# Kernel tuning notes

Measured on AMD Instinct MI355X. Metric: run time of the kernel, lower is better.

Reference implementation:

```python
import jax, jax.numpy as jnp
import numpy as np

N_NODES = 100000
N_EDGES = 1600000
N_GRAPHS = 512
IN_DIM = 128
HID = 128
N_CLASSES = 10


def _gcn_conv(x, W, b, src, dst, n):
    """PyG GCNConv: out = D^{-1/2} (A+I) D^{-1/2} (x @ W) + b."""
    xw = x @ W  # [n, out_dim]
    loop = jnp.arange(n)
    s = jnp.concatenate([src, loop])  # add self loops
    d = jnp.concatenate([dst, loop])
    deg = jax.ops.segment_sum(jnp.ones(s.shape, dtype=xw.dtype), d, num_segments=n)
    dinv = jnp.where(deg > 0, jax.lax.rsqrt(deg), jnp.zeros((), xw.dtype))
    norm = dinv[s] * dinv[d]  # [E + n]
    out = jax.ops.segment_sum(xw[s] * norm[:, None], d, num_segments=n)
    return out + b


def _global_mean_pool(x, batch, num_graphs):
    sums = jax.ops.segment_sum(x, batch, num_segments=num_graphs)
    cnts = jax.ops.segment_sum(jnp.ones(batch.shape, dtype=x.dtype), batch, num_segments=num_graphs)
    return sums / jnp.maximum(cnts, 1.0)[:, None]


def setup_inputs() -> dict:
    key = jax.random.key(0)
    ks = jax.random.split(key, 8)
    x = jax.random.normal(ks[0], (N_NODES, IN_DIM), dtype=jnp.float32)
    edge_index = jax.random.randint(ks[1], (2, N_EDGES), 0, N_NODES, dtype=jnp.int64)
    batch = jnp.sort(jax.random.randint(ks[2], (N_NODES,), 0, N_GRAPHS, dtype=jnp.int64))
    sc = 1.0 / np.sqrt(IN_DIM)
    W1 = jax.random.normal(ks[3], (IN_DIM, HID), dtype=jnp.float32) * sc
    b1 = jnp.zeros((HID,), dtype=jnp.float32)
    W2 = jax.random.normal(ks[4], (HID, HID), dtype=jnp.float32) * (1.0 / np.sqrt(HID))
    b2 = jnp.zeros((HID,), dtype=jnp.float32)
    Wc = jax.random.normal(ks[5], (HID, N_CLASSES), dtype=jnp.float32) * (1.0 / np.sqrt(HID))
    bc = jnp.zeros((N_CLASSES,), dtype=jnp.float32)
    return {"x": x, "edge_index": edge_index, "batch": batch,
            "W1": W1, "b1": b1, "W2": W2, "b2": b2, "Wc": Wc, "bc": bc}


def reference(x, edge_index, batch, W1, b1, W2, b2, Wc, bc):
    src, dst = edge_index[0], edge_index[1]
    n = x.shape[0]
    h = _gcn_conv(x, W1, b1, src, dst, n)
    h = jax.nn.relu(h)
    h = _gcn_conv(h, W2, b2, src, dst, n)
    g = _global_mean_pool(h, batch, N_GRAPHS)
    return g @ Wc + bc
```

## Files before the change

### kernel.cpp

```cpp
#include <hip/hip_runtime.h>

#define N_NODES 100000
#define N_EDGES 1600000
#define N_GRAPHS 512
#define DIM 128
#define NCLS 10
#define NBKT 782
#define BCAP 2560

typedef __attribute__((ext_vector_type(8))) short short8;
typedef __attribute__((ext_vector_type(4))) float f32x4;

static __device__ __forceinline__ unsigned short f2bf(float f) {
    unsigned u = __float_as_uint(f);
    unsigned r = (u + 0x7FFF + ((u >> 16) & 1)) >> 16;
    return (unsigned short)r;
}
static __device__ __forceinline__ float bf2f(unsigned u) {
    return __uint_as_float(u << 16);
}


__global__ void k_wprep(const float* __restrict__ W1, const float* __restrict__ W2,
                        unsigned short* __restrict__ wf1, unsigned short* __restrict__ wf2,
                        int* __restrict__ bcnt) {
    int b = blockIdx.x;
    if (b >= 128) {
        int i = (b - 128) * 256 + threadIdx.x;
        if (i < NBKT) bcnt[i] = 0;
        return;
    }
    const float* W = (b < 64) ? W1 : W2;
    unsigned short* wfrag = (b < 64) ? wf1 : wf2;
    int t = (b & 63) * 256 + threadIdx.x;
    int j = t & 7, lane = (t >> 3) & 63, nt = (t >> 9) & 7, kit = t >> 12;
    int k = kit * 32 + (lane >> 4) * 8 + j;
    int n = nt * 16 + (lane & 15);
    float v = W[k * 128 + n];
    unsigned short h = f2bf(v);
    wfrag[t] = h;
    wfrag[16384 + t] = f2bf(v - bf2f(h));
}


__global__ __launch_bounds__(256) void k_bucket(
    const int* __restrict__ src, const int* __restrict__ dst,
    int* __restrict__ bcnt, unsigned* __restrict__ bpack, int E) {
    __shared__ int cnt[NBKT];
    __shared__ int base[NBKT];
    int tid = threadIdx.x;
    for (int i = tid; i < NBKT; i += 256) cnt[i] = 0;
    __syncthreads();
    int e0 = blockIdx.x * 4096 + tid;
    unsigned pk[16]; short bk[16];
#pragma unroll
    for (int j = 0; j < 16; j++) {
        int e = e0 + j * 256;
        if (e < E) {
            int s = src[e], d = dst[e];
            bk[j] = (short)(d >> 7);
            pk[j] = ((unsigned)(d & 127) << 17) | (unsigned)s;
            atomicAdd(&cnt[bk[j]], 1);
        } else bk[j] = -1;
    }
    __syncthreads();
    for (int i = tid; i < NBKT; i += 256) {
        int c = cnt[i];
        base[i] = c ? atomicAdd(&bcnt[i], c) : 0;
        cnt[i] = 0;
    }
    __syncthreads();
#pragma unroll
    for (int j = 0; j < 16; j++) {
        if (bk[j] >= 0) {
            int p = base[bk[j]] + atomicAdd(&cnt[bk[j]], 1);
            if (p < BCAP) bpack[(size_t)bk[j] * BCAP + p] = pk[j];
        }
    }
}


static __device__ __forceinline__ void bsort_body(
    char* smemraw, int b,
    const unsigned* __restrict__ bpack, const int* __restrict__ bcnt,
    int* __restrict__ rp, float* __restrict__ dinv,
    int* __restrict__ esrc, int N, float* __restrict__ dvs) {
    int* lds      = (int*)smemraw;
    int* cnt      = lds + 256;
    int* scan     = lds + 384;
    int* cur      = lds + 512;
    int* gbase_sh = lds + 640;
    int tid = threadIdx.x;
    int v[4], pre[4];
    int s = 0;
#pragma unroll
    for (int j = 0; j < 4; j++) {
        int idx = tid * 4 + j;
        v[j] = (idx < NBKT) ? min(bcnt[idx], BCAP) : 0;
        pre[j] = s; s += v[j];
    }
    lds[tid] = s;
    __syncthreads();
    for (int off = 1; off < 256; off <<= 1) {
        int t = (tid >= off) ? lds[tid - off] : 0;
        __syncthreads();
        lds[tid] += t;
        __syncthreads();
    }
    if (tid == (b >> 2)) *gbase_sh = lds[tid] - s + pre[b & 3];
    if (tid < 128) cnt[tid] = 0;
    __syncthreads();
    int gbase = *gbase_sh;
    int n0 = b << 7;
    int m = min(bcnt[b], BCAP);
    const unsigned* bp = bpack + (size_t)b * BCAP;
    for (int j = tid; j < m; j += 256) atomicAdd(&cnt[bp[j] >> 17], 1);
    __syncthreads();
    if (tid < 128) scan[tid] = cnt[tid];
    __syncthreads();
    for (int off = 1; off < 128; off <<= 1) {
        int t = (tid < 128 && tid >= off) ? scan[tid - off] : 0;
        __syncthreads();
        if (tid < 128) scan[tid] += t;
        __syncthreads();
    }
    if (tid < 128) {
        int c = cnt[tid];
        int excl = scan[tid] - c;
        int node = n0 + tid;
        float dv = rsqrtf((float)(c + 1));
        if (node <= N) rp[node] = gbase + excl;
        if (node < N) dinv[node] = dv;
        dvs[tid] = dv;
        cur[tid] = gbase + excl;
    }
    __syncthreads();
    for (int j = tid; j < m; j += 256) {
        unsigned pk = bp[j];
        int p = atomicAdd(&cur[pk >> 17], 1);
        esrc[p] = (int)(pk & 0x1FFFF);
    }
}

static __device__ __forceinline__ void gemm_f32_body(
    char* smemraw, int rowBlk,
    const float* __restrict__ A, const unsigned short* __restrict__ wfrag,
    const float* __restrict__ dvs, unsigned short* __restrict__ ybf, int M) {
    unsigned short* ldsw = (unsigned short*)smemraw;
    int tid = threadIdx.x, wave = tid >> 6, lane = tid & 63;
    int m = lane & 15, quad = lane >> 4;
    int rowBase = rowBlk * 128 + wave * 32;
    int r0 = rowBase + m, r1 = rowBase + 16 + m;
    for (int i = tid; i < 2048; i += 256)
        ((short8*)ldsw)[i] = ((const short8*)wfrag)[i];
    __syncthreads();
    f32x4 acc0[8], acc1[8];
#pragma unroll
    for (int i = 0; i < 8; i++) { acc0[i] = (f32x4){0,0,0,0}; acc1[i] = (f32x4){0,0,0,0}; }
    const unsigned short* wlo = wfrag + 16384;

#pragma unroll
    for (int kit = 0; kit < 4; kit++) {
        float a0[8], a1[8];
        if (r0 < M) {
            const float4* ap = (const float4*)(A + (size_t)r0 * 128 + kit * 32 + quad * 8);
            float4 f0 = ap[0], f1 = ap[1];
            a0[0]=f0.x; a0[1]=f0.y; a0[2]=f0.z; a0[3]=f0.w; a0[4]=f1.x; a0[5]=f1.y; a0[6]=f1.z; a0[7]=f1.w;
        } else { for (int j = 0; j < 8; j++) a0[j] = 0.f; }
        if (r1 < M) {
            const float4* ap = (const float4*)(A + (size_t)r1 * 128 + kit * 32 + quad * 8);
            float4 f0 = ap[0], f1 = ap[1];
            a1[0]=f0.x; a1[1]=f0.y; a1[2]=f0.z; a1[3]=f0.w; a1[4]=f1.x; a1[5]=f1.y; a1[6]=f1.z; a1[7]=f1.w;
        } else { for (int j = 0; j < 8; j++) a1[j] = 0.f; }
        short8 ahi0, alo0, ahi1, alo1;
#pragma unroll
        for (int j = 0; j < 8; j++) {
            unsigned short h0 = f2bf(a0[j]);
            ahi0[j] = (short)h0; alo0[j] = (short)f2bf(a0[j] - bf2f(h0));
            unsigned short h1 = f2bf(a1[j]);
            ahi1[j] = (short)h1; alo1[j] = (short)f2bf(a1[j] - bf2f(h1));
        }
        int fb = kit * 4096 + lane * 8;
#pragma unroll
        for (int nt = 0; nt < 8; nt++) {
            int idx = fb + nt * 512;
            short8 bhi = *(const short8*)(ldsw + idx);
            short8 blo = *(const short8*)(wlo + idx);
            acc0[nt] = __builtin_amdgcn_mfma_f32_16x16x32_bf16(ahi0, bhi, acc0[nt], 0, 0, 0);
            acc0[nt] = __builtin_amdgcn_mfma_f32_16x16x32_bf16(alo0, bhi, acc0[nt], 0, 0, 0);
            acc0[nt] = __builtin_amdgcn_mfma_f32_16x16x32_bf16(ahi0, blo, acc0[nt], 0, 0, 0);
            acc1[nt] = __builtin_amdgcn_mfma_f32_16x16x32_bf16(ahi1, bhi, acc1[nt], 0, 0, 0);
            acc1[nt] = __builtin_amdgcn_mfma_f32_16x16x32_bf16(alo1, bhi, acc1[nt], 0, 0, 0);
            acc1[nt] = __builtin_amdgcn_mfma_f32_16x16x32_bf16(ahi1, blo, acc1[nt], 0, 0, 0);
        }
    }
    __syncthreads();
    unsigned short* wsm = ldsw + wave * 32 * 136;
#pragma unroll
    for (int rg = 0; rg < 4; rg++) {
        float s0 = dvs[wave * 32 + quad * 4 + rg];
        float s1 = dvs[wave * 32 + 16 + quad * 4 + rg];
#pragma unroll
        for (int nt = 0; nt < 8; nt++) {
            wsm[(quad * 4 + rg) * 136 + nt * 16 + m] = f2bf(acc0[nt][rg] * s0);
            wsm[(16 + quad * 4 + rg) * 136 + nt * 16 + m] = f2bf(acc1[nt][rg] * s1);
        }
    }
    __syncthreads();
#pragma unroll
    for (int i = 0; i < 8; i++) {
        int rl = i * 4 + quad;
        int grow = rowBase + rl;
        if (grow < M) {
            short8 v = *(const short8*)(wsm + rl * 136 + m * 8);
            *(short8*)(ybf + (size_t)grow * 128 + m * 8) = v;
        }
    }
}


__global__ __launch_bounds__(256) void k_fuse(
    const unsigned* __restrict__ bpack, const int* __restrict__ bcnt,
    int* __restrict__ rp, float* __restrict__ dinv, int* __restrict__ esrc, int N,
    const float* __restrict__ A, const unsigned short* __restrict__ wfrag,
    unsigned short* __restrict__ ybf, int M) {
    __shared__ __align__(16) char smem[4 * 32 * 136 * 2];
    __shared__ float dvs[128];
    int b = blockIdx.x;
    bsort_body(smem, b, bpack, bcnt, rp, dinv, esrc, N, dvs);
    __syncthreads();
    gemm_f32_body(smem, b, A, wfrag, dvs, ybf, M);
}


__global__ __launch_bounds__(256) void k_gemm_bf(
    const unsigned short* __restrict__ A, const unsigned short* __restrict__ wfrag,
    const float* __restrict__ dinv, unsigned short* __restrict__ ybf, int M) {
    __shared__ unsigned short ldsw[4 * 32 * 136];
    int tid = threadIdx.x, wave = tid >> 6, lane = tid & 63;
    int m = lane & 15, quad = lane >> 4;
    int rowBase = blockIdx.x * 128 + wave * 32;
    int r0 = rowBase + m, r1 = rowBase + 16 + m;
    for (int i = tid; i < 2048; i += 256)
        ((short8*)ldsw)[i] = ((const short8*)wfrag)[i];
    __syncthreads();
    f32x4 acc0[8], acc1[8];
#pragma unroll
    for (int i = 0; i < 8; i++) { acc0[i] = (f32x4){0,0,0,0}; acc1[i] = (f32x4){0,0,0,0}; }
    const unsigned short* wlo = wfrag + 16384;

#pragma unroll
    for (int kit = 0; kit < 4; kit++) {
        short8 ah0, ah1;
        if (r0 < M) ah0 = *(const short8*)(A + (size_t)r0 * 128 + kit * 32 + quad * 8);
        else { for (int j = 0; j < 8; j++) ah0[j] = 0; }
        if (r1 < M) ah1 = *(const short8*)(A + (size_t)r1 * 128 + kit * 32 + quad * 8);
        else { for (int j = 0; j < 8; j++) ah1[j] = 0; }
        int fb = kit * 4096 + lane * 8;
#pragma unroll
        for (int nt = 0; nt < 8; nt++) {
            int idx = fb + nt * 512;
            short8 bhi = *(const short8*)(ldsw + idx);
            short8 blo = *(const short8*)(wlo + idx);
            acc0[nt] = __builtin_amdgcn_mfma_f32_16x16x32_bf16(ah0, bhi, acc0[nt], 0, 0, 0);
            acc0[nt] = __builtin_amdgcn_mfma_f32_16x16x32_bf16(ah0, blo, acc0[nt], 0, 0, 0);
            acc1[nt] = __builtin_amdgcn_mfma_f32_16x16x32_bf16(ah1, bhi, acc1[nt], 0, 0, 0);
            acc1[nt] = __builtin_amdgcn_mfma_f32_16x16x32_bf16(ah1, blo, acc1[nt], 0, 0, 0);
        }
    }
    __syncthreads();
    float dv0 = (r0 < M) ? dinv[r0] : 0.f;
    float dv1 = (r1 < M) ? dinv[r1] : 0.f;
    unsigned short* wsm = ldsw + wave * 32 * 136;
#pragma unroll
    for (int rg = 0; rg < 4; rg++) {
        float s0 = __shfl(dv0, quad * 4 + rg);
        float s1 = __shfl(dv1, quad * 4 + rg);
#pragma unroll
        for (int nt = 0; nt < 8; nt++) {
            wsm[(quad * 4 + rg) * 136 + nt * 16 + m] = f2bf(acc0[nt][rg] * s0);
            wsm[(16 + quad * 4 + rg) * 136 + nt * 16 + m] = f2bf(acc1[nt][rg] * s1);
        }
    }
    __syncthreads();
#pragma unroll
    for (int i = 0; i < 8; i++) {
        int rl = i * 4 + quad;
        int grow = rowBase + rl;
        if (grow < M) {
            short8 v = *(const short8*)(wsm + rl * 136 + m * 8);
            *(short8*)(ybf + (size_t)grow * 128 + m * 8) = v;
        }
    }
}


__global__ __launch_bounds__(256) void k_agg(
    const unsigned short* __restrict__ y, const float* __restrict__ dinv,
    const int* __restrict__ rp, const int* __restrict__ esrc,
    const float* __restrict__ bias, unsigned* __restrict__ out, int relu, int N) {
    int wave = threadIdx.x >> 6;
    int lane = threadIdx.x & 63;
    int node = blockIdx.x * 4 + wave;
    if (node >= N) return;
    const unsigned* y2 = (const unsigned*)y;
    unsigned vs = y2[(size_t)node * 64 + lane];
    float a0 = bf2f(vs & 0xFFFF), a1 = bf2f(vs >> 16);
    int beg = rp[node], end = rp[node + 1];
    int j = beg;
    while (j < end) {
        int idxv = (j + lane < end) ? esrc[j + lane] : 0;
        int cnt = end - j; if (cnt > 64) cnt = 64;
        int i = 0;
        for (; i + 4 <= cnt; i += 4) {
            int s0 = __shfl(idxv, i + 0);
            int s1 = __shfl(idxv, i + 1);
            int s2 = __shfl(idxv, i + 2);
            int s3 = __shfl(idxv, i + 3);
            unsigned v0 = y2[(size_t)s0 * 64 + lane];
            unsigned v1 = y2[(size_t)s1 * 64 + lane];
            unsigned v2 = y2[(size_t)s2 * 64 + lane];
            unsigned v3 = y2[(size_t)s3 * 64 + lane];
            a0 += bf2f(v0 & 0xFFFF); a1 += bf2f(v0 >> 16);
            a0 += bf2f(v1 & 0xFFFF); a1 += bf2f(v1 >> 16);
            a0 += bf2f(v2 & 0xFFFF); a1 += bf2f(v2 >> 16);
            a0 += bf2f(v3 & 0xFFFF); a1 += bf2f(v3 >> 16);
        }
        for (; i < cnt; i++) {
            int s = __shfl(idxv, i);
            unsigned v = y2[(size_t)s * 64 + lane];
            a0 += bf2f(v & 0xFFFF); a1 += bf2f(v >> 16);
        }
        j += cnt;
    }
    float s = dinv[node];
    float2 bv = ((const float2*)bias)[lane];
    float o0 = s * a0 + bv.x;
    float o1 = s * a1 + bv.y;
    if (relu) { o0 = fmaxf(o0, 0.f); o1 = fmaxf(o1, 0.f); }
    out[(size_t)node * 64 + lane] = (unsigned)f2bf(o0) | ((unsigned)f2bf(o1) << 16);
}


__global__ __launch_bounds__(256) void k_poolhead(
    const unsigned* __restrict__ h2, const int* __restrict__ batch,
    const float* __restrict__ Wc, const float* __restrict__ bc,
    float* __restrict__ out, int n) {
    __shared__ float2 red[4][64];
    __shared__ float grow[DIM];
    int gid = blockIdx.x;
    int tid = threadIdx.x, wave = tid >> 6, lane = tid & 63;
    int lo = 0, hi = n;
    while (lo < hi) { int mid = (lo + hi) >> 1; if (batch[mid] < gid) lo = mid + 1; else hi = mid; }
    int start = lo;
    hi = n;
    while (lo < hi) { int mid = (lo + hi) >> 1; if (batch[mid] < gid + 1) lo = mid + 1; else hi = mid; }
    int end = lo;
    float a0 = 0.f, a1 = 0.f;
    for (int r = start + wave; r < end; r += 4) {
        unsigned v = h2[(size_t)r * 64 + lane];
        a0 += bf2f(v & 0xFFFF); a1 += bf2f(v >> 16);
    }
    red[wave][lane] = make_float2(a0, a1);
    __syncthreads();
    if (tid < 64) {
        float2 s = red[0][tid];
        s.x += red[1][tid].x; s.y += red[1][tid].y;
        s.x += red[2][tid].x; s.y += red[2][tid].y;
        s.x += red[3][tid].x; s.y += red[3][tid].y;
        int cnt = end - start;
        float inv = 1.f / (float)(cnt > 0 ? cnt : 1);
        grow[tid * 2] = s.x * inv;
        grow[tid * 2 + 1] = s.y * inv;
    }
    __syncthreads();
    if (tid < NCLS) {
        float acc = bc[tid];
#pragma unroll 16
        for (int k = 0; k < DIM; k++) acc += grow[k] * Wc[k * NCLS + tid];
        out[gid * NCLS + tid] = acc;
    }
}

extern "C" void kernel_launch(void* const* d_in, const int* in_sizes, int n_in,
                              void* d_out, int out_size, void* d_ws, size_t ws_size,
                              hipStream_t stream) {
    const float* x    = (const float*)d_in[0];
    const int*   ei   = (const int*)d_in[1];
    const int*   batch= (const int*)d_in[2];
    const float* W1   = (const float*)d_in[3];
    const float* b1   = (const float*)d_in[4];
    const float* W2   = (const float*)d_in[5];
    const float* b2   = (const float*)d_in[6];
    const float* Wc   = (const float*)d_in[7];
    const float* bc   = (const float*)d_in[8];
    float* out = (float*)d_out;
    const int N = N_NODES, E = N_EDGES;
    const int* src = ei;
    const int* dst = ei + E;

    char* ws = (char*)d_ws;
    size_t off = 0;
    auto carve = [&](size_t bytes) -> void* {
        void* p = ws + off;
        off = (off + bytes + 255) & ~(size_t)255;
        return p;
    };
    int*      rp    = (int*)     carve((size_t)(N + 1) * 4);
    float*    dinv  = (float*)   carve((size_t)N * 4);
    int*      bcnt  = (int*)     carve(NBKT * 4);
    unsigned* bpack = (unsigned*)carve((size_t)NBKT * BCAP * 4);
    int*      esrc  = (int*)     carve((size_t)E * 4);
    unsigned short* wf1 = (unsigned short*)carve(2 * 16384 * 2);
    unsigned short* wf2 = (unsigned short*)carve(2 * 16384 * 2);
    unsigned short* bufY = (unsigned short*)carve((size_t)N * DIM * 2);
    unsigned short* bufH = (unsigned short*)carve((size_t)N * DIM * 2);
    (void)ws_size; (void)n_in; (void)in_sizes; (void)out_size;

    const int nbBkt = (E + 4095) / 4096;
    const int gemmGrid = (N + 127) / 128;

    hipLaunchKernelGGL(k_wprep,  dim3(128 + (NBKT + 255) / 256), dim3(256), 0, stream, W1, W2, wf1, wf2, bcnt);
    hipLaunchKernelGGL(k_bucket, dim3(nbBkt), dim3(256), 0, stream, src, dst, bcnt, bpack, E);
    hipLaunchKernelGGL(k_fuse, dim3(NBKT), dim3(256), 0, stream,
                       bpack, bcnt, rp, dinv, esrc, N, x, wf1, bufY, N);
    hipLaunchKernelGGL(k_agg, dim3((N + 3) / 4), dim3(256), 0, stream, bufY, dinv, rp, esrc, b1, (unsigned*)bufH, 1, N);
    hipLaunchKernelGGL(k_gemm_bf, dim3(gemmGrid), dim3(256), 0, stream, bufH, wf2, dinv, bufY, N);
    hipLaunchKernelGGL(k_agg, dim3((N + 3) / 4), dim3(256), 0, stream, bufY, dinv, rp, esrc, b2, (unsigned*)bufH, 0, N);
    hipLaunchKernelGGL(k_poolhead, dim3(N_GRAPHS), dim3(256), 0, stream, (const unsigned*)bufH, batch, Wc, bc, out, N);
}
```

Measured before the change: 337.7 us.

## Fuse layer-1 aggregation with layer-2 GEMM in one slab kernel

Replaces the separate layer-1 aggregation kernel and the layer-2 bf16 GEMM with one kernel. Each block of 8 waves gathers neighbor features for 128 nodes, applies bias and ReLU, and writes the rows to LDS as bf16. The same block then runs the MFMA GEMM against W2 straight from LDS and scales each row by dinv. This removes a global write and read of the hidden activation and one launch. In exchange, the irregular gather and the GEMM are serialized within a block, the grid has only 782 blocks, and LDS use per block is larger, which can lower occupancy for the latency-bound gather.

```diff
diff --git a/kernel.cpp b/kernel.cpp
--- a/kernel.cpp
+++ b/kernel.cpp
@@ -233,61 +233,100 @@
 }
 
 
-__global__ __launch_bounds__(256) void k_gemm_bf(
-    const unsigned short* __restrict__ A, const unsigned short* __restrict__ wfrag,
-    const float* __restrict__ dinv, unsigned short* __restrict__ ybf, int M) {
-    __shared__ unsigned short ldsw[4 * 32 * 136];
+__global__ __launch_bounds__(512) void k_aggemm(
+    const unsigned short* __restrict__ y, const float* __restrict__ dinv,
+    const int* __restrict__ rp, const int* __restrict__ esrc,
+    const float* __restrict__ bias, const unsigned short* __restrict__ wfrag,
+    unsigned short* __restrict__ ybf, int N) {
+    __shared__ unsigned short h1[128 * 136];
+    __shared__ unsigned short ldsw[16384];
+    __shared__ float dvs[128];
     int tid = threadIdx.x, wave = tid >> 6, lane = tid & 63;
+    int slab = blockIdx.x * 128;
+
+    for (int i = tid; i < 2048; i += 512)
+        ((short8*)ldsw)[i] = ((const short8*)wfrag)[i];
+
+    const unsigned* y2 = (const unsigned*)y;
+    float2 bv = ((const float2*)bias)[lane];
+    for (int i = 0; i < 16; i++) {
+        int local = wave * 16 + i;
+        int node = slab + local;
+        unsigned packed = 0;
+        float sd = 0.f;
+        if (node < N) {
+            sd = dinv[node];
+            unsigned vs = y2[(size_t)node * 64 + lane];
+            float a0 = bf2f(vs & 0xFFFF), a1 = bf2f(vs >> 16);
+            int beg = rp[node], end = rp[node + 1];
+            int j = beg;
+            while (j < end) {
+                int idxv = (j + lane < end) ? esrc[j + lane] : 0;
+                int cnt = end - j; if (cnt > 64) cnt = 64;
+                int ii = 0;
+                for (; ii + 4 <= cnt; ii += 4) {
+                    int s0 = __shfl(idxv, ii + 0);
+                    int s1 = __shfl(idxv, ii + 1);
+                    int s2 = __shfl(idxv, ii + 2);
+                    int s3 = __shfl(idxv, ii + 3);
+                    unsigned v0 = y2[(size_t)s0 * 64 + lane];
+                    unsigned v1 = y2[(size_t)s1 * 64 + lane];
+                    unsigned v2 = y2[(size_t)s2 * 64 + lane];
+                    unsigned v3 = y2[(size_t)s3 * 64 + lane];
+                    a0 += bf2f(v0 & 0xFFFF); a1 += bf2f(v0 >> 16);
+                    a0 += bf2f(v1 & 0xFFFF); a1 += bf2f(v1 >> 16);
+                    a0 += bf2f(v2 & 0xFFFF); a1 += bf2f(v2 >> 16);
+                    a0 += bf2f(v3 & 0xFFFF); a1 += bf2f(v3 >> 16);
+                }
+                for (; ii < cnt; ii++) {
+                    int s = __shfl(idxv, ii);
+                    unsigned v = y2[(size_t)s * 64 + lane];
+                    a0 += bf2f(v & 0xFFFF); a1 += bf2f(v >> 16);
+                }
+                j += cnt;
+            }
+            float o0 = fmaxf(sd * a0 + bv.x, 0.f);
+            float o1 = fmaxf(sd * a1 + bv.y, 0.f);
+            packed = (unsigned)f2bf(o0) | ((unsigned)f2bf(o1) << 16);
+        }
+        *(unsigned*)&h1[local * 136 + lane * 2] = packed;
+        if (lane == 0) dvs[local] = sd;
+    }
+    __syncthreads();
+
     int m = lane & 15, quad = lane >> 4;
-    int rowBase = blockIdx.x * 128 + wave * 32;
-    int r0 = rowBase + m, r1 = rowBase + 16 + m;
-    for (int i = tid; i < 2048; i += 256)
-        ((short8*)ldsw)[i] = ((const short8*)wfrag)[i];
-    __syncthreads();
-    f32x4 acc0[8], acc1[8];
-#pragma unroll
-    for (int i = 0; i < 8; i++) { acc0[i] = (f32x4){0,0,0,0}; acc1[i] = (f32x4){0,0,0,0}; }
+    int rowLocal = wave * 16;
+    f32x4 acc[8];
+#pragma unroll
+    for (int i = 0; i < 8; i++) acc[i] = (f32x4){0,0,0,0};
     const unsigned short* wlo = wfrag + 16384;
-
 #pragma unroll
     for (int kit = 0; kit < 4; kit++) {
-        short8 ah0, ah1;
-        if (r0 < M) ah0 = *(const short8*)(A + (size_t)r0 * 128 + kit * 32 + quad * 8);
-        else { for (int j = 0; j < 8; j++) ah0[j] = 0; }
-        if (r1 < M) ah1 = *(const short8*)(A + (size_t)r1 * 128 + kit * 32 + quad * 8);
-        else { for (int j = 0; j < 8; j++) ah1[j] = 0; }
+        short8 ah = *(const short8*)(h1 + (rowLocal + m) * 136 + kit * 32 + quad * 8);
         int fb = kit * 4096 + lane * 8;
 #pragma unroll
         for (int nt = 0; nt < 8; nt++) {
             int idx = fb + nt * 512;
             short8 bhi = *(const short8*)(ldsw + idx);
             short8 blo = *(const short8*)(wlo + idx);
-            acc0[nt] = __builtin_amdgcn_mfma_f32_16x16x32_bf16(ah0, bhi, acc0[nt], 0, 0, 0);
-            acc0[nt] = __builtin_amdgcn_mfma_f32_16x16x32_bf16(ah0, blo, acc0[nt], 0, 0, 0);
-            acc1[nt] = __builtin_amdgcn_mfma_f32_16x16x32_bf16(ah1, bhi, acc1[nt], 0, 0, 0);
-            acc1[nt] = __builtin_amdgcn_mfma_f32_16x16x32_bf16(ah1, blo, acc1[nt], 0, 0, 0);
-        }
-    }
-    __syncthreads();
-    float dv0 = (r0 < M) ? dinv[r0] : 0.f;
-    float dv1 = (r1 < M) ? dinv[r1] : 0.f;
-    unsigned short* wsm = ldsw + wave * 32 * 136;
+            acc[nt] = __builtin_amdgcn_mfma_f32_16x16x32_bf16(ah, bhi, acc[nt], 0, 0, 0);
+            acc[nt] = __builtin_amdgcn_mfma_f32_16x16x32_bf16(ah, blo, acc[nt], 0, 0, 0);
+        }
+    }
+    unsigned short* wsm = h1 + rowLocal * 136;
 #pragma unroll
     for (int rg = 0; rg < 4; rg++) {
-        float s0 = __shfl(dv0, quad * 4 + rg);
-        float s1 = __shfl(dv1, quad * 4 + rg);
+        float s0 = dvs[rowLocal + quad * 4 + rg];
 #pragma unroll
         for (int nt = 0; nt < 8; nt++) {
-            wsm[(quad * 4 + rg) * 136 + nt * 16 + m] = f2bf(acc0[nt][rg] * s0);
-            wsm[(16 + quad * 4 + rg) * 136 + nt * 16 + m] = f2bf(acc1[nt][rg] * s1);
-        }
-    }
-    __syncthreads();
-#pragma unroll
-    for (int i = 0; i < 8; i++) {
+            wsm[(quad * 4 + rg) * 136 + nt * 16 + m] = f2bf(acc[nt][rg] * s0);
+        }
+    }
+#pragma unroll
+    for (int i = 0; i < 4; i++) {
         int rl = i * 4 + quad;
-        int grow = rowBase + rl;
-        if (grow < M) {
+        int grow = slab + rowLocal + rl;
+        if (grow < N) {
             short8 v = *(const short8*)(wsm + rl * 136 + m * 8);
             *(short8*)(ybf + (size_t)grow * 128 + m * 8) = v;
         }
@@ -418,14 +457,13 @@
     (void)ws_size; (void)n_in; (void)in_sizes; (void)out_size;
 
     const int nbBkt = (E + 4095) / 4096;
-    const int gemmGrid = (N + 127) / 128;
 
     hipLaunchKernelGGL(k_wprep,  dim3(128 + (NBKT + 255) / 256), dim3(256), 0, stream, W1, W2, wf1, wf2, bcnt);
     hipLaunchKernelGGL(k_bucket, dim3(nbBkt), dim3(256), 0, stream, src, dst, bcnt, bpack, E);
     hipLaunchKernelGGL(k_fuse, dim3(NBKT), dim3(256), 0, stream,
                        bpack, bcnt, rp, dinv, esrc, N, x, wf1, bufY, N);
-    hipLaunchKernelGGL(k_agg, dim3((N + 3) / 4), dim3(256), 0, stream, bufY, dinv, rp, esrc, b1, (unsigned*)bufH, 1, N);
-    hipLaunchKernelGGL(k_gemm_bf, dim3(gemmGrid), dim3(256), 0, stream, bufH, wf2, dinv, bufY, N);
-    hipLaunchKernelGGL(k_agg, dim3((N + 3) / 4), dim3(256), 0, stream, bufY, dinv, rp, esrc, b2, (unsigned*)bufH, 0, N);
-    hipLaunchKernelGGL(k_poolhead, dim3(N_GRAPHS), dim3(256), 0, stream, (const unsigned*)bufH, batch, Wc, bc, out, N);
-}
+    hipLaunchKernelGGL(k_aggemm, dim3(NBKT), dim3(512), 0, stream,
+                       bufY, dinv, rp, esrc, b1, wf2, bufH, N);
+    hipLaunchKernelGGL(k_agg, dim3((N + 3) / 4), dim3(256), 0, stream, bufH, dinv, rp, esrc, b2, (unsigned*)bufY, 0, N);
+    hipLaunchKernelGGL(k_poolhead, dim3(N_GRAPHS), dim3(256), 0, stream, (const unsigned*)bufY, batch, Wc, bc, out, N);
+}
```

Result: slower. 359.6 us (+6.5%).

## Store GEMM output in column-slab layout and split aggregation by feature slice

Applied to the files above, without the earlier changes.

The GEMM kernels now write the bf16 feature matrix as 8 column slabs of 16 features each, so each slab is 32 bytes per node. The aggregation kernel gives each block one slab and 32 nodes, with 8 edges gathered at once per wave, and reduces the partial sums across lanes with shuffles. The aim is that each slab (about 3.2MB) fits in cache, improving locality of the random gathers. In exchange, edge indices are re-read for every slice and each gather is narrower, and the output is written with nontemporal stores.

```diff
diff --git a/kernel.cpp b/kernel.cpp
--- a/kernel.cpp
+++ b/kernel.cpp
@@ -7,6 +7,9 @@
 #define NCLS 10
 #define NBKT 782
 #define BCAP 2560
+#define NPAD (NBKT * 128)
+#define SLABU32 ((size_t)NPAD * 8)
+#define SLABUS  ((size_t)NPAD * 16)
 
 typedef __attribute__((ext_vector_type(8))) short short8;
 typedef __attribute__((ext_vector_type(4))) float f32x4;
@@ -213,7 +216,7 @@
         int grow = rowBase + rl;
         if (grow < M) {
             short8 v = *(const short8*)(wsm + rl * 136 + m * 8);
-            *(short8*)(ybf + (size_t)grow * 128 + m * 8) = v;
+            *(short8*)(ybf + (size_t)(m >> 1) * SLABUS + (size_t)grow * 16 + (m & 1) * 8) = v;
         }
     }
 }
@@ -289,7 +292,7 @@
         int grow = rowBase + rl;
         if (grow < M) {
             short8 v = *(const short8*)(wsm + rl * 136 + m * 8);
-            *(short8*)(ybf + (size_t)grow * 128 + m * 8) = v;
+            *(short8*)(ybf + (size_t)(m >> 1) * SLABUS + (size_t)grow * 16 + (m & 1) * 8) = v;
         }
     }
 }
@@ -299,46 +302,57 @@
     const unsigned short* __restrict__ y, const float* __restrict__ dinv,
     const int* __restrict__ rp, const int* __restrict__ esrc,
     const float* __restrict__ bias, unsigned* __restrict__ out, int relu, int N) {
-    int wave = threadIdx.x >> 6;
-    int lane = threadIdx.x & 63;
-    int node = blockIdx.x * 4 + wave;
-    if (node >= N) return;
-    const unsigned* y2 = (const unsigned*)y;
-    unsigned vs = y2[(size_t)node * 64 + lane];
-    float a0 = bf2f(vs & 0xFFFF), a1 = bf2f(vs >> 16);
-    int beg = rp[node], end = rp[node + 1];
-    int j = beg;
-    while (j < end) {
-        int idxv = (j + lane < end) ? esrc[j + lane] : 0;
-        int cnt = end - j; if (cnt > 64) cnt = 64;
-        int i = 0;
-        for (; i + 4 <= cnt; i += 4) {
-            int s0 = __shfl(idxv, i + 0);
-            int s1 = __shfl(idxv, i + 1);
-            int s2 = __shfl(idxv, i + 2);
-            int s3 = __shfl(idxv, i + 3);
-            unsigned v0 = y2[(size_t)s0 * 64 + lane];
-            unsigned v1 = y2[(size_t)s1 * 64 + lane];
-            unsigned v2 = y2[(size_t)s2 * 64 + lane];
-            unsigned v3 = y2[(size_t)s3 * 64 + lane];
-            a0 += bf2f(v0 & 0xFFFF); a1 += bf2f(v0 >> 16);
-            a0 += bf2f(v1 & 0xFFFF); a1 += bf2f(v1 >> 16);
-            a0 += bf2f(v2 & 0xFFFF); a1 += bf2f(v2 >> 16);
-            a0 += bf2f(v3 & 0xFFFF); a1 += bf2f(v3 >> 16);
-        }
-        for (; i < cnt; i++) {
-            int s = __shfl(idxv, i);
-            unsigned v = y2[(size_t)s * 64 + lane];
-            a0 += bf2f(v & 0xFFFF); a1 += bf2f(v >> 16);
-        }
-        j += cnt;
-    }
-    float s = dinv[node];
-    float2 bv = ((const float2*)bias)[lane];
-    float o0 = s * a0 + bv.x;
-    float o1 = s * a1 + bv.y;
-    if (relu) { o0 = fmaxf(o0, 0.f); o1 = fmaxf(o1, 0.f); }
-    out[(size_t)node * 64 + lane] = (unsigned)f2bf(o0) | ((unsigned)f2bf(o1) << 16);
+    int tid = threadIdx.x, wave = tid >> 6, lane = tid & 63;
+    int slice = blockIdx.x & 7;
+    int chunk = blockIdx.x >> 3;
+    int nodeBase = chunk * 32 + wave * 8;
+    const unsigned* ys = (const unsigned*)y + (size_t)slice * SLABU32;
+    int dp = lane & 7;
+    int slot = lane >> 3;
+    int col = slice * 8 + dp;
+    float2 bq = ((const float2*)bias)[col];
+#pragma unroll 1
+    for (int ni = 0; ni < 8; ni++) {
+        int node = nodeBase + ni;
+        if (node >= N) return;
+        int beg = rp[node], end = rp[node + 1];
+        float a0 = 0.f, a1 = 0.f;
+        int j = beg;
+        while (j < end) {
+            int idxv = (j + lane < end) ? esrc[j + lane] : 0;
+            int cnt = end - j; if (cnt > 64) cnt = 64;
+            int g = 0;
+            for (; g + 16 <= cnt; g += 16) {
+                int s0 = __shfl(idxv, g + slot);
+                int s1 = __shfl(idxv, g + 8 + slot);
+                unsigned v0 = ys[(size_t)s0 * 8 + dp];
+                unsigned v1 = ys[(size_t)s1 * 8 + dp];
+                a0 += bf2f(v0 & 0xFFFF); a1 += bf2f(v0 >> 16);
+                a0 += bf2f(v1 & 0xFFFF); a1 += bf2f(v1 >> 16);
+            }
+            for (; g < cnt; g += 8) {
+                int idxe = g + slot;
+                int s = __shfl(idxv, idxe);
+                unsigned v = 0;
+                if (idxe < cnt) v = ys[(size_t)s * 8 + dp];
+                a0 += bf2f(v & 0xFFFF); a1 += bf2f(v >> 16);
+            }
+            j += cnt;
+        }
+        a0 += __shfl_xor(a0, 8);  a1 += __shfl_xor(a1, 8);
+        a0 += __shfl_xor(a0, 16); a1 += __shfl_xor(a1, 16);
+        a0 += __shfl_xor(a0, 32); a1 += __shfl_xor(a1, 32);
+        if (slot == 0) {
+            unsigned vs = ys[(size_t)node * 8 + dp];
+            a0 += bf2f(vs & 0xFFFF); a1 += bf2f(vs >> 16);
+            float sdv = dinv[node];
+            float o0 = sdv * a0 + bq.x;
+            float o1 = sdv * a1 + bq.y;
+            if (relu) { o0 = fmaxf(o0, 0.f); o1 = fmaxf(o1, 0.f); }
+            unsigned pv = (unsigned)f2bf(o0) | ((unsigned)f2bf(o1) << 16);
+            __builtin_nontemporal_store(pv, &out[(size_t)node * 64 + col]);
+        }
+    }
 }
 
 
@@ -413,19 +427,20 @@
     int*      esrc  = (int*)     carve((size_t)E * 4);
     unsigned short* wf1 = (unsigned short*)carve(2 * 16384 * 2);
     unsigned short* wf2 = (unsigned short*)carve(2 * 16384 * 2);
-    unsigned short* bufY = (unsigned short*)carve((size_t)N * DIM * 2);
+    unsigned short* bufY = (unsigned short*)carve((size_t)NPAD * DIM * 2);
     unsigned short* bufH = (unsigned short*)carve((size_t)N * DIM * 2);
     (void)ws_size; (void)n_in; (void)in_sizes; (void)out_size;
 
     const int nbBkt = (E + 4095) / 4096;
     const int gemmGrid = (N + 127) / 128;
+    const int aggGrid = ((N + 31) / 32) * 8;
 
     hipLaunchKernelGGL(k_wprep,  dim3(128 + (NBKT + 255) / 256), dim3(256), 0, stream, W1, W2, wf1, wf2, bcnt);
     hipLaunchKernelGGL(k_bucket, dim3(nbBkt), dim3(256), 0, stream, src, dst, bcnt, bpack, E);
     hipLaunchKernelGGL(k_fuse, dim3(NBKT), dim3(256), 0, stream,
                        bpack, bcnt, rp, dinv, esrc, N, x, wf1, bufY, N);
-    hipLaunchKernelGGL(k_agg, dim3((N + 3) / 4), dim3(256), 0, stream, bufY, dinv, rp, esrc, b1, (unsigned*)bufH, 1, N);
+    hipLaunchKernelGGL(k_agg, dim3(aggGrid), dim3(256), 0, stream, bufY, dinv, rp, esrc, b1, (unsigned*)bufH, 1, N);
     hipLaunchKernelGGL(k_gemm_bf, dim3(gemmGrid), dim3(256), 0, stream, bufH, wf2, dinv, bufY, N);
-    hipLaunchKernelGGL(k_agg, dim3((N + 3) / 4), dim3(256), 0, stream, bufY, dinv, rp, esrc, b2, (unsigned*)bufH, 0, N);
+    hipLaunchKernelGGL(k_agg, dim3(aggGrid), dim3(256), 0, stream, bufY, dinv, rp, esrc, b2, (unsigned*)bufH, 0, N);
     hipLaunchKernelGGL(k_poolhead, dim3(N_GRAPHS), dim3(256), 0, stream, (const unsigned*)bufH, batch, Wc, bc, out, N);
 }
```

Result: slower. 572.9 us (+69.6%).
